# Kernel optimization log

Measured on AMD Instinct MI355X. Metric: run time of the kernel, lower is better.

The kernel has to match this reference:

```python
import jax, jax.numpy as jnp
import numpy as np

B, D_IN, D_H = 4096, 1024, 2048


def setup_inputs() -> dict:
    key = jax.random.key(0)
    ks = jax.random.split(key, 16)
    s_in = 1.0 / np.sqrt(D_IN)
    s_h = 1.0 / np.sqrt(D_H)
    inp = {
        "x": jax.random.normal(ks[0], (B, D_IN), jnp.float32),
        "h_prev": jax.random.normal(ks[1], (B, D_H), jnp.float32),
        "c_prev": jax.random.normal(ks[2], (B, D_H), jnp.float32),
        "n_prev": jax.random.uniform(ks[3], (B, D_H), jnp.float32) + 0.5,
        # input-gate weights [D_H, D_IN] (torch Linear layout) + biases
        "Wz": jax.random.uniform(ks[4], (D_H, D_IN), jnp.float32, -s_in, s_in),
        "Wi": jax.random.uniform(ks[5], (D_H, D_IN), jnp.float32, -s_in, s_in),
        "Wf": jax.random.uniform(ks[6], (D_H, D_IN), jnp.float32, -s_in, s_in),
        "Wo": jax.random.uniform(ks[7], (D_H, D_IN), jnp.float32, -s_in, s_in),
        "bz": jax.random.uniform(ks[8], (D_H,), jnp.float32, -s_in, s_in),
        "bi": jax.random.uniform(ks[9], (D_H,), jnp.float32, -s_in, s_in),
        "bf": jax.random.uniform(ks[10], (D_H,), jnp.float32, -s_in, s_in),
        "bo": jax.random.uniform(ks[11], (D_H,), jnp.float32, -s_in, s_in),
        # recurrent weights [D_H, D_H], bias-free
        "Rz": jax.random.uniform(ks[12], (D_H, D_H), jnp.float32, -s_h, s_h),
        "Ri": jax.random.uniform(ks[13], (D_H, D_H), jnp.float32, -s_h, s_h),
        "Rf": jax.random.uniform(ks[14], (D_H, D_H), jnp.float32, -s_h, s_h),
        "Ro": jax.random.uniform(ks[15], (D_H, D_H), jnp.float32, -s_h, s_h),
    }
    return inp


def reference(x, h_prev, c_prev, n_prev,
              Wz, Wi, Wf, Wo, bz, bi, bf, bo,
              Rz, Ri, Rf, Ro):
    # Fuse the 4 input GEMMs and 4 recurrent GEMMs into two batched contractions.
    Wcat = jnp.concatenate([Wz, Wi, Wf, Wo], axis=0)      # [4H, D_IN]
    Rcat = jnp.concatenate([Rz, Ri, Rf, Ro], axis=0)      # [4H, H]
    bcat = jnp.concatenate([bz, bi, bf, bo], axis=0)      # [4H]
    pre = x @ Wcat.T + h_prev @ Rcat.T + bcat              # [B, 4H]
    az, ai, af, ao = jnp.split(pre, 4, axis=1)
    z = jnp.tanh(az)
    i = jnp.exp(ai)
    f = jnp.exp(af)
    o = jax.nn.sigmoid(ao)
    c = f * c_prev + i * z
    n = f * n_prev + i
    h = o * (c / n)
    return h
```

## Files before the change

### kernel.cpp

```cpp
#include <hip/hip_runtime.h>
#include <hip/hip_fp16.h>

#define B_SZ  4096
#define DIN   1024
#define DH    2048
#define K_TOT 3072
#define N_TOT 8192

#define BM 128
#define BN 128
#define BK 32

typedef _Float16 half8 __attribute__((ext_vector_type(8)));
typedef _Float16 half4 __attribute__((ext_vector_type(4)));
typedef float   float4v __attribute__((ext_vector_type(4)));

__device__ __forceinline__ void load_lds16(const void* g, void* l) {
    __builtin_amdgcn_global_load_lds(
        (const __attribute__((address_space(1))) void*)g,
        (__attribute__((address_space(3))) void*)l,
        16, 0, 0);
}

__global__ __launch_bounds__(256) void cast_A_kernel(
        const float* __restrict__ x, const float* __restrict__ h,
        _Float16* __restrict__ A) {
    int idx = (blockIdx.x * 256 + threadIdx.x) * 4;
    int b = idx / K_TOT;
    int c = idx - b * K_TOT;
    const float* src = (c < DIN) ? (x + b * DIN + c) : (h + b * DH + (c - DIN));
    float4 v = *reinterpret_cast<const float4*>(src);
    half4 o;
    o.x = (_Float16)v.x; o.y = (_Float16)v.y;
    o.z = (_Float16)v.z; o.w = (_Float16)v.w;
    *reinterpret_cast<half4*>(A + idx) = o;
}

__global__ __launch_bounds__(256) void cast_W_kernel(
        const float* __restrict__ Wz, const float* __restrict__ Wi,
        const float* __restrict__ Wf, const float* __restrict__ Wo,
        const float* __restrict__ Rz, const float* __restrict__ Ri,
        const float* __restrict__ Rf, const float* __restrict__ Ro,
        _Float16* __restrict__ Wb) {
    int idx = (blockIdx.x * 256 + threadIdx.x) * 4;
    int n = idx / K_TOT;
    int c = idx - n * K_TOT;
    int g = (n >> 5) & 3;
    int j = ((n >> 7) << 5) | (n & 31);
    const float* W = (g == 0) ? Wz : (g == 1) ? Wi : (g == 2) ? Wf : Wo;
    const float* R = (g == 0) ? Rz : (g == 1) ? Ri : (g == 2) ? Rf : Ro;
    const float* src = (c < DIN) ? (W + j * DIN + c) : (R + j * DH + (c - DIN));
    float4 v = *reinterpret_cast<const float4*>(src);
    half4 o;
    o.x = (_Float16)v.x; o.y = (_Float16)v.y;
    o.z = (_Float16)v.z; o.w = (_Float16)v.w;
    *reinterpret_cast<half4*>(Wb + idx) = o;
}

__global__ __launch_bounds__(256) void slstm_gemm_kernel(
        const _Float16* __restrict__ A, const _Float16* __restrict__ Wb,
        const float* __restrict__ c_prev, const float* __restrict__ n_prev,
        const float* __restrict__ bz, const float* __restrict__ bi,
        const float* __restrict__ bf, const float* __restrict__ bo,
        float* __restrict__ Hout) {
    __shared__ __align__(16) _Float16 As[BM * BK];
    __shared__ __align__(16) _Float16 Bs[BN * BK];

    const int ntile = blockIdx.x;
    const int mtile = blockIdx.y;
    const int tid  = threadIdx.x;
    const int wv   = tid >> 6;
    const int l    = tid & 63;
    const int quad = l >> 4;
    const int l16  = l & 15;

    const int m0 = mtile * BM;
    const int n0 = ntile * BN;

    float4v acc[2][8];
#pragma unroll
    for (int i = 0; i < 2; i++)
#pragma unroll
        for (int j = 0; j < 8; j++) acc[i][j] = (float4v){0.f, 0.f, 0.f, 0.f};

    const int chunk0 = wv * 2;
    const int srow0  = chunk0 * 16 + (l >> 2);
    const int srow1  = srow0 + 16;
    const int skoff  = (l & 3) * 8;

    const _Float16* Ag0 = A  + (size_t)(m0 + srow0) * K_TOT + skoff;
    const _Float16* Ag1 = A  + (size_t)(m0 + srow1) * K_TOT + skoff;
    const _Float16* Bg0 = Wb + (size_t)(n0 + srow0) * K_TOT + skoff;
    const _Float16* Bg1 = Wb + (size_t)(n0 + srow1) * K_TOT + skoff;

    _Float16* AsL0 = As + chunk0 * 512;
    _Float16* AsL1 = As + (chunk0 + 1) * 512;
    _Float16* BsL0 = Bs + chunk0 * 512;
    _Float16* BsL1 = Bs + (chunk0 + 1) * 512;

    for (int kt = 0; kt < K_TOT; kt += BK) {
        load_lds16(Ag0 + kt, AsL0);
        load_lds16(Ag1 + kt, AsL1);
        load_lds16(Bg0 + kt, BsL0);
        load_lds16(Bg1 + kt, BsL1);
        __syncthreads();

        half8 afr0 = *reinterpret_cast<const half8*>(As + (wv * 32 + l16) * BK + quad * 8);
        half8 afr1 = *reinterpret_cast<const half8*>(As + (wv * 32 + 16 + l16) * BK + quad * 8);
        half8 bfr[8];
#pragma unroll
        for (int nf = 0; nf < 8; nf++)
            bfr[nf] = *reinterpret_cast<const half8*>(Bs + (nf * 16 + l16) * BK + quad * 8);

#pragma unroll
        for (int nf = 0; nf < 8; nf++) {
            acc[0][nf] = __builtin_amdgcn_mfma_f32_16x16x32_f16(afr0, bfr[nf], acc[0][nf], 0, 0, 0);
            acc[1][nf] = __builtin_amdgcn_mfma_f32_16x16x32_f16(afr1, bfr[nf], acc[1][nf], 0, 0, 0);
        }
        __syncthreads();
    }

    const int j_base = ntile * 32;
#pragma unroll
    for (int nf = 0; nf < 2; nf++) {
        const int j = j_base + nf * 16 + l16;
        const float bzv = bz[j], biv = bi[j], bfv = bf[j], bov = bo[j];
#pragma unroll
        for (int mf = 0; mf < 2; mf++) {
#pragma unroll
            for (int r = 0; r < 4; r++) {
                const int row = m0 + wv * 32 + mf * 16 + quad * 4 + r;
                const size_t off = (size_t)row * DH + j;
                float az  = acc[mf][nf][r]     + bzv;
                float ai  = acc[mf][nf + 2][r] + biv;
                float af_ = acc[mf][nf + 4][r] + bfv;
                float ao  = acc[mf][nf + 6][r] + bov;
                float z  = tanhf(az);
                float iv = __expf(ai);
                float fv = __expf(af_);
                float ov = 1.0f / (1.0f + __expf(-ao));
                float cc = fv * c_prev[off] + iv * z;
                float nn = fv * n_prev[off] + iv;
                Hout[off] = ov * (cc / nn);
            }
        }
    }
}

extern "C" void kernel_launch(void* const* d_in, const int* in_sizes, int n_in,
                              void* d_out, int out_size, void* d_ws, size_t ws_size,
                              hipStream_t stream) {
    const float* x      = (const float*)d_in[0];
    const float* h_prev = (const float*)d_in[1];
    const float* c_prev = (const float*)d_in[2];
    const float* n_prev = (const float*)d_in[3];
    const float* Wz = (const float*)d_in[4];
    const float* Wi = (const float*)d_in[5];
    const float* Wf = (const float*)d_in[6];
    const float* Wo = (const float*)d_in[7];
    const float* bz = (const float*)d_in[8];
    const float* bi = (const float*)d_in[9];
    const float* bf = (const float*)d_in[10];
    const float* bo = (const float*)d_in[11];
    const float* Rz = (const float*)d_in[12];
    const float* Ri = (const float*)d_in[13];
    const float* Rf = (const float*)d_in[14];
    const float* Ro = (const float*)d_in[15];

    _Float16* A  = (_Float16*)d_ws;
    _Float16* Wb = A + (size_t)B_SZ * K_TOT;

    cast_A_kernel<<<(B_SZ * K_TOT / 4) / 256, 256, 0, stream>>>(x, h_prev, A);
    cast_W_kernel<<<(N_TOT * K_TOT / 4) / 256, 256, 0, stream>>>(
        Wz, Wi, Wf, Wo, Rz, Ri, Rf, Ro, Wb);

    dim3 grid(N_TOT / BN, B_SZ / BM);
    slstm_gemm_kernel<<<grid, 256, 0, stream>>>(
        A, Wb, c_prev, n_prev, bz, bi, bf, bo, (float*)d_out);
}
```

Before: 516.9 us.

## Use 2x2 warp tiling in GEMM with matching weight interleave and wider casts

The GEMM warp layout changes from each wave owning 32 rows by 128 columns to a 2x2 grid of waves, each owning 64x64. The weight-row interleave in the cast kernel is reordered so each wave's 64 columns hold all four gates for 16 hidden units, keeping the fused epilogue local to the wave. This cuts LDS fragment reads per wave from 10 to 8 per k-step. The cast kernels now handle 8 elements per thread, and the epilogue uses fast-divide and exp-based tanh, giving up some accuracy.

```diff
diff --git a/kernel.cpp b/kernel.cpp
--- a/kernel.cpp
+++ b/kernel.cpp
@@ -12,7 +12,6 @@
 #define BK 32
 
 typedef _Float16 half8 __attribute__((ext_vector_type(8)));
-typedef _Float16 half4 __attribute__((ext_vector_type(4)));
 typedef float   float4v __attribute__((ext_vector_type(4)));
 
 __device__ __forceinline__ void load_lds16(const void* g, void* l) {
@@ -25,15 +24,19 @@
 __global__ __launch_bounds__(256) void cast_A_kernel(
         const float* __restrict__ x, const float* __restrict__ h,
         _Float16* __restrict__ A) {
-    int idx = (blockIdx.x * 256 + threadIdx.x) * 4;
+    int idx = (blockIdx.x * 256 + threadIdx.x) * 8;
     int b = idx / K_TOT;
     int c = idx - b * K_TOT;
-    const float* src = (c < DIN) ? (x + b * DIN + c) : (h + b * DH + (c - DIN));
-    float4 v = *reinterpret_cast<const float4*>(src);
-    half4 o;
-    o.x = (_Float16)v.x; o.y = (_Float16)v.y;
-    o.z = (_Float16)v.z; o.w = (_Float16)v.w;
-    *reinterpret_cast<half4*>(A + idx) = o;
+    const float* src = (c < DIN) ? (x + (size_t)b * DIN + c)
+                                 : (h + (size_t)b * DH + (c - DIN));
+    float4 v0 = *reinterpret_cast<const float4*>(src);
+    float4 v1 = *reinterpret_cast<const float4*>(src + 4);
+    half8 o;
+    o[0] = (_Float16)v0.x; o[1] = (_Float16)v0.y;
+    o[2] = (_Float16)v0.z; o[3] = (_Float16)v0.w;
+    o[4] = (_Float16)v1.x; o[5] = (_Float16)v1.y;
+    o[6] = (_Float16)v1.z; o[7] = (_Float16)v1.w;
+    *reinterpret_cast<half8*>(A + idx) = o;
 }
 
 __global__ __launch_bounds__(256) void cast_W_kernel(
@@ -42,19 +45,24 @@
         const float* __restrict__ Rz, const float* __restrict__ Ri,
         const float* __restrict__ Rf, const float* __restrict__ Ro,
         _Float16* __restrict__ Wb) {
-    int idx = (blockIdx.x * 256 + threadIdx.x) * 4;
+    int idx = (blockIdx.x * 256 + threadIdx.x) * 8;
     int n = idx / K_TOT;
     int c = idx - n * K_TOT;
-    int g = (n >> 5) & 3;
-    int j = ((n >> 7) << 5) | (n & 31);
+    int t = n & 127;
+    int g = (t >> 4) & 3;
+    int j = ((n >> 7) << 5) + ((t >> 6) << 4) + (t & 15);
     const float* W = (g == 0) ? Wz : (g == 1) ? Wi : (g == 2) ? Wf : Wo;
     const float* R = (g == 0) ? Rz : (g == 1) ? Ri : (g == 2) ? Rf : Ro;
-    const float* src = (c < DIN) ? (W + j * DIN + c) : (R + j * DH + (c - DIN));
-    float4 v = *reinterpret_cast<const float4*>(src);
-    half4 o;
-    o.x = (_Float16)v.x; o.y = (_Float16)v.y;
-    o.z = (_Float16)v.z; o.w = (_Float16)v.w;
-    *reinterpret_cast<half4*>(Wb + idx) = o;
+    const float* src = (c < DIN) ? (W + (size_t)j * DIN + c)
+                                 : (R + (size_t)j * DH + (c - DIN));
+    float4 v0 = *reinterpret_cast<const float4*>(src);
+    float4 v1 = *reinterpret_cast<const float4*>(src + 4);
+    half8 o;
+    o[0] = (_Float16)v0.x; o[1] = (_Float16)v0.y;
+    o[2] = (_Float16)v0.z; o[3] = (_Float16)v0.w;
+    o[4] = (_Float16)v1.x; o[5] = (_Float16)v1.y;
+    o[6] = (_Float16)v1.z; o[7] = (_Float16)v1.w;
+    *reinterpret_cast<half8*>(Wb + idx) = o;
 }
 
 __global__ __launch_bounds__(256) void slstm_gemm_kernel(
@@ -70,6 +78,8 @@
     const int mtile = blockIdx.y;
     const int tid  = threadIdx.x;
     const int wv   = tid >> 6;
+    const int wm   = wv >> 1;
+    const int wn   = wv & 1;
     const int l    = tid & 63;
     const int quad = l >> 4;
     const int l16  = l & 15;
@@ -77,11 +87,11 @@
     const int m0 = mtile * BM;
     const int n0 = ntile * BN;
 
-    float4v acc[2][8];
+    float4v acc[4][4];
 #pragma unroll
-    for (int i = 0; i < 2; i++)
+    for (int i = 0; i < 4; i++)
 #pragma unroll
-        for (int j = 0; j < 8; j++) acc[i][j] = (float4v){0.f, 0.f, 0.f, 0.f};
+        for (int j = 0; j < 4; j++) acc[i][j] = (float4v){0.f, 0.f, 0.f, 0.f};
 
     const int chunk0 = wv * 2;
     const int srow0  = chunk0 * 16 + (l >> 2);
@@ -105,44 +115,44 @@
         load_lds16(Bg1 + kt, BsL1);
         __syncthreads();
 
-        half8 afr0 = *reinterpret_cast<const half8*>(As + (wv * 32 + l16) * BK + quad * 8);
-        half8 afr1 = *reinterpret_cast<const half8*>(As + (wv * 32 + 16 + l16) * BK + quad * 8);
-        half8 bfr[8];
+        half8 afr[4], bfr[4];
 #pragma unroll
-        for (int nf = 0; nf < 8; nf++)
-            bfr[nf] = *reinterpret_cast<const half8*>(Bs + (nf * 16 + l16) * BK + quad * 8);
+        for (int mf = 0; mf < 4; mf++)
+            afr[mf] = *reinterpret_cast<const half8*>(As + (wm * 64 + mf * 16 + l16) * BK + quad * 8);
+#pragma unroll
+        for (int nf = 0; nf < 4; nf++)
+            bfr[nf] = *reinterpret_cast<const half8*>(Bs + (wn * 64 + nf * 16 + l16) * BK + quad * 8);
 
 #pragma unroll
-        for (int nf = 0; nf < 8; nf++) {
-            acc[0][nf] = __builtin_amdgcn_mfma_f32_16x16x32_f16(afr0, bfr[nf], acc[0][nf], 0, 0, 0);
-            acc[1][nf] = __builtin_amdgcn_mfma_f32_16x16x32_f16(afr1, bfr[nf], acc[1][nf], 0, 0, 0);
-        }
+        for (int mf = 0; mf < 4; mf++)
+#pragma unroll
+            for (int nf = 0; nf < 4; nf++)
+                acc[mf][nf] = __builtin_amdgcn_mfma_f32_16x16x32_f16(afr[mf], bfr[nf], acc[mf][nf], 0, 0, 0);
         __syncthreads();
     }
 
-    const int j_base = ntile * 32;
+    const int j = ntile * 32 + wn * 16 + l16;
+    const float bzv = bz[j], biv = bi[j], bfv = bf[j], bov = bo[j];
 #pragma unroll
-    for (int nf = 0; nf < 2; nf++) {
-        const int j = j_base + nf * 16 + l16;
-        const float bzv = bz[j], biv = bi[j], bfv = bf[j], bov = bo[j];
+    for (int mf = 0; mf < 4; mf++) {
 #pragma unroll
-        for (int mf = 0; mf < 2; mf++) {
-#pragma unroll
-            for (int r = 0; r < 4; r++) {
-                const int row = m0 + wv * 32 + mf * 16 + quad * 4 + r;
-                const size_t off = (size_t)row * DH + j;
-                float az  = acc[mf][nf][r]     + bzv;
-                float ai  = acc[mf][nf + 2][r] + biv;
-                float af_ = acc[mf][nf + 4][r] + bfv;
-                float ao  = acc[mf][nf + 6][r] + bov;
-                float z  = tanhf(az);
-                float iv = __expf(ai);
-                float fv = __expf(af_);
-                float ov = 1.0f / (1.0f + __expf(-ao));
-                float cc = fv * c_prev[off] + iv * z;
-                float nn = fv * n_prev[off] + iv;
-                Hout[off] = ov * (cc / nn);
-            }
+        for (int r = 0; r < 4; r++) {
+            const int row = m0 + wm * 64 + mf * 16 + quad * 4 + r;
+            const size_t off = (size_t)row * DH + j;
+            const float az  = acc[mf][0][r] + bzv;
+            const float ai  = acc[mf][1][r] + biv;
+            const float af_ = acc[mf][2][r] + bfv;
+            const float ao  = acc[mf][3][r] + bov;
+            const float ax = fabsf(az);
+            const float e2 = __expf(-2.0f * ax);
+            float tz = __fdividef(1.0f - e2, 1.0f + e2);
+            tz = (az >= 0.0f) ? tz : -tz;
+            const float iv = __expf(ai);
+            const float fv = __expf(af_);
+            const float ov = __fdividef(1.0f, 1.0f + __expf(-ao));
+            const float cc = fv * c_prev[off] + iv * tz;
+            const float nn = fv * n_prev[off] + iv;
+            Hout[off] = ov * __fdividef(cc, nn);
         }
     }
 }
@@ -170,8 +180,8 @@
     _Float16* A  = (_Float16*)d_ws;
     _Float16* Wb = A + (size_t)B_SZ * K_TOT;
 
-    cast_A_kernel<<<(B_SZ * K_TOT / 4) / 256, 256, 0, stream>>>(x, h_prev, A);
-    cast_W_kernel<<<(N_TOT * K_TOT / 4) / 256, 256, 0, stream>>>(
+    cast_A_kernel<<<(B_SZ * K_TOT / 8) / 256, 256, 0, stream>>>(x, h_prev, A);
+    cast_W_kernel<<<(N_TOT * K_TOT / 8) / 256, 256, 0, stream>>>(
         Wz, Wi, Wf, Wo, Rz, Ri, Rf, Ro, Wb);
 
     dim3 grid(N_TOT / BN, B_SZ / BM);
```

After: 480.8 us. 7.0% less time.
